# Optimization experiments

Hardware: AMD Instinct MI355X
Metric: run time of the kernel (lower is better)

Reference implementation:

```python
import jax, jax.numpy as jnp
import numpy as np

B = 8192   # particle ensemble (vmapped y0)
T = 64     # timesteps
D = 2      # data_size
W = 128    # width_size
CAP = 5.0  # cap() clamps trajectories to a bounded domain


def setup_inputs() -> dict:
    key = jax.random.key(0)
    ks = jax.random.split(key, 10)
    s_in = 1.0 / np.sqrt(D)
    s_h = 1.0 / np.sqrt(W)
    u = jax.random.uniform
    return {
        "ts": jnp.linspace(0.0, 1.0, T, dtype=jnp.float32),
        "y0": jax.random.normal(ks[0], (B, D), jnp.float32),
        "W1": u(ks[1], (W, D), jnp.float32, -s_in, s_in),
        "b1": u(ks[2], (W,), jnp.float32, -s_in, s_in),
        "W2": u(ks[3], (W, W), jnp.float32, -s_h, s_h),
        "b2": u(ks[4], (W,), jnp.float32, -s_h, s_h),
        "W3": u(ks[5], (W, W), jnp.float32, -s_h, s_h),
        "b3": u(ks[6], (W,), jnp.float32, -s_h, s_h),
        "W4": u(ks[7], (D, W), jnp.float32, -s_h, s_h),
        "b4": u(ks[8], (D,), jnp.float32, -s_h, s_h),
    }


def _func(y, W1, b1, W2, b2, W3, b3, W4, b4):
    # eqx.nn.MLP(data_size -> data_size, width_size, depth=3),
    # activation=leaky_relu, final_activation=identity. y: [B, D]
    h = jax.nn.leaky_relu(y @ W1.T + b1)
    h = jax.nn.leaky_relu(h @ W2.T + b2)
    h = jax.nn.leaky_relu(h @ W3.T + b3)
    return h @ W4.T + b4


def reference(ts, y0, W1, b1, W2, b2, W3, b3, W4, b4):
    # MultiTerm(drift, ODETerm(func)) with Euler on the uniform grid ts:
    #   y_{n+1} = y_n + dt_n * (drift(t_n, y_n) + func(t_n, y_n))
    # drift vector field: f(t, y) = -y
    dts = ts[1:] - ts[:-1]  # [T-1]

    def step(y, dt):
        dy = -y + _func(y, W1, b1, W2, b2, W3, b3, W4, b4)
        y_new = y + dt * dy
        return y_new, y_new

    _, ys_tail = jax.lax.scan(step, y0, dts)          # [T-1, B, D]
    ys = jnp.concatenate([y0[None], ys_tail], axis=0)  # [T, B, D] == solution.ys
    return jnp.clip(ys, -CAP, CAP)  # cap(solution.ys)
```

## Files before the change

kernel.cpp:

```cpp
#include <hip/hip_runtime.h>

#define NB 8192
#define NT 64
#define FCAP 5.0f

typedef unsigned int u32;
typedef float f32x4 __attribute__((ext_vector_type(4)));
typedef __bf16 bf16x8 __attribute__((ext_vector_type(8)));
typedef u32 u32x4 __attribute__((ext_vector_type(4)));
typedef u32 u32x2 __attribute__((ext_vector_type(2)));

static __device__ __forceinline__ u32 pk2(float lo, float hi) {
  u32 r;
  asm("v_cvt_pk_bf16_f32 %0, %1, %2" : "=v"(r) : "v"(lo), "v"(hi));
  return r;
}
static __device__ __forceinline__ float clipc(float a) { return fminf(fmaxf(a, -FCAP), FCAP); }

static __device__ __forceinline__ bf16x8 mkfrag(const float* __restrict__ p) {
  f32x4 a = *(const f32x4*)p, b = *(const f32x4*)(p + 4);
  u32x4 wv = {pk2(a[0], a[1]), pk2(a[2], a[3]), pk2(b[0], b[1]), pk2(b[2], b[3])};
  return __builtin_bit_cast(bf16x8, wv);
}

#define MFMA16(A, B, C) __builtin_amdgcn_mfma_f32_16x16x32_bf16(A, B, C, 0, 0, 0)

static __device__ __forceinline__ f32x4 lrelu4(f32x4 v) {
  return __builtin_elementwise_max(v, v * 0.01f);
}


__global__ __launch_bounds__(256, 2) void ode_kernel(
    const float* __restrict__ ts, const float* __restrict__ y0,
    const float* __restrict__ W1, const float* __restrict__ b1,
    const float* __restrict__ W2, const float* __restrict__ b2,
    const float* __restrict__ W3, const float* __restrict__ b3,
    const float* __restrict__ W4, const float* __restrict__ b4,
    float* __restrict__ out) {
  const int tid = threadIdx.x;
  const int wv = __builtin_amdgcn_readfirstlane(tid >> 6);
  const int l = tid & 63;
  const int g = l >> 4;
  const int c = l & 15;
  const int gp0 = blockIdx.x * 16;

  __shared__ alignas(16) u32 bufA[16 * 68];
  __shared__ alignas(16) u32 bufB[16 * 68];
  __shared__ alignas(16) float fbuf[16 * 20];

  bf16x8 aW2[2][4], aW3[2][4];
#pragma unroll
  for (int mt = 0; mt < 2; ++mt) {
    const int R = 32 * wv + 16 * mt + c;
#pragma unroll
    for (int kt = 0; kt < 4; ++kt) {
      aW2[mt][kt] = mkfrag(W2 + R * 128 + 32 * kt + 8 * g);
      aW3[mt][kt] = mkfrag(W3 + R * 128 + 32 * kt + 8 * g);
    }
  }
  bf16x8 aW1[2];
#pragma unroll
  for (int mt = 0; mt < 2; ++mt) {
    const int R = 32 * wv + 16 * mt + c;
    u32x4 f = {0, 0, 0, 0};
    if (g == 0) {
      f[0] = pk2(W1[2 * R], W1[2 * R + 1]);
      f[1] = pk2(b1[R], 0.f);
    }
    aW1[mt] = __builtin_bit_cast(bf16x8, f);
  }
  bf16x8 aW4;
  {
    u32x4 f = {0, 0, 0, 0};
    if (c < 2) {
      const float* s = W4 + c * 128 + 32 * wv + 8 * g;
      f32x4 a = *(const f32x4*)s, b = *(const f32x4*)(s + 4);
      f = (u32x4){pk2(a[0], a[1]), pk2(a[2], a[3]), pk2(b[0], b[1]), pk2(b[2], b[3])};
    }
    aW4 = __builtin_bit_cast(bf16x8, f);
  }
  f32x4 cb2[2], cb3[2];
#pragma unroll
  for (int mt = 0; mt < 2; ++mt) {
#pragma unroll
    for (int r = 0; r < 4; ++r) {
      const int row = 32 * wv + 16 * mt + 4 * g + r;
      cb2[mt][r] = b2[row];
      cb3[mt][r] = b3[row];
    }
  }
  const float b40 = b4[0], b41 = b4[1];

  float y1 = y0[(gp0 + c) * 2];
  float y2 = y0[(gp0 + c) * 2 + 1];

  if (wv == 0 && g == 0) {
    float2 st = {clipc(y1), clipc(y2)};
    *(float2*)(out + (gp0 + c) * 2) = st;
  }

  const f32x4 zero4 = {0.f, 0.f, 0.f, 0.f};
  const int wbase = 68 * c + 16 * wv + 2 * g;
  const int rbase = 68 * c + 4 * g;

#pragma unroll 1
  for (int t = 0; t < NT - 1; ++t) {
    const float dt = ts[t + 1] - ts[t];

    u32x4 byw = {0, 0, 0, 0};
    if (g == 0) {
      byw[0] = pk2(y1, y2);
      byw[1] = 0x3f80u;
    }
    const bf16x8 By = __builtin_bit_cast(bf16x8, byw);
    f32x4 C0 = lrelu4(MFMA16(aW1[0], By, zero4));
    f32x4 C1 = lrelu4(MFMA16(aW1[1], By, zero4));
    *(__shared__ u32x2*)&bufA[wbase]     = (u32x2){pk2(C0[0], C0[1]), pk2(C0[2], C0[3])};
    *(__shared__ u32x2*)&bufA[wbase + 8] = (u32x2){pk2(C1[0], C1[1]), pk2(C1[2], C1[3])};
    __syncthreads();

    {
      const bf16x8 q0 = __builtin_bit_cast(bf16x8, *(const __shared__ u32x4*)&bufA[rbase]);
      const bf16x8 q1 = __builtin_bit_cast(bf16x8, *(const __shared__ u32x4*)&bufA[rbase + 16]);
      const bf16x8 q2 = __builtin_bit_cast(bf16x8, *(const __shared__ u32x4*)&bufA[rbase + 32]);
      const bf16x8 q3 = __builtin_bit_cast(bf16x8, *(const __shared__ u32x4*)&bufA[rbase + 48]);
      f32x4 D0 = MFMA16(aW2[0][0], q0, cb2[0]);
      f32x4 D1 = MFMA16(aW2[1][0], q0, cb2[1]);
      f32x4 E0 = MFMA16(aW2[0][1], q1, zero4);
      f32x4 E1 = MFMA16(aW2[1][1], q1, zero4);
      D0 = MFMA16(aW2[0][2], q2, D0);
      D1 = MFMA16(aW2[1][2], q2, D1);
      E0 = MFMA16(aW2[0][3], q3, E0);
      E1 = MFMA16(aW2[1][3], q3, E1);
      C0 = lrelu4(D0 + E0);
      C1 = lrelu4(D1 + E1);
    }
    *(__shared__ u32x2*)&bufB[wbase]     = (u32x2){pk2(C0[0], C0[1]), pk2(C0[2], C0[3])};
    *(__shared__ u32x2*)&bufB[wbase + 8] = (u32x2){pk2(C1[0], C1[1]), pk2(C1[2], C1[3])};
    __syncthreads();

    {
      const bf16x8 q0 = __builtin_bit_cast(bf16x8, *(const __shared__ u32x4*)&bufB[rbase]);
      const bf16x8 q1 = __builtin_bit_cast(bf16x8, *(const __shared__ u32x4*)&bufB[rbase + 16]);
      const bf16x8 q2 = __builtin_bit_cast(bf16x8, *(const __shared__ u32x4*)&bufB[rbase + 32]);
      const bf16x8 q3 = __builtin_bit_cast(bf16x8, *(const __shared__ u32x4*)&bufB[rbase + 48]);
      f32x4 D0 = MFMA16(aW3[0][0], q0, cb3[0]);
      f32x4 D1 = MFMA16(aW3[1][0], q0, cb3[1]);
      f32x4 E0 = MFMA16(aW3[0][1], q1, zero4);
      f32x4 E1 = MFMA16(aW3[1][1], q1, zero4);
      D0 = MFMA16(aW3[0][2], q2, D0);
      D1 = MFMA16(aW3[1][2], q2, D1);
      E0 = MFMA16(aW3[0][3], q3, E0);
      E1 = MFMA16(aW3[1][3], q3, E1);
      C0 = lrelu4(D0 + E0);
      C1 = lrelu4(D1 + E1);
    }
    *(__shared__ u32x2*)&bufA[wbase]     = (u32x2){pk2(C0[0], C0[1]), pk2(C0[2], C0[3])};
    *(__shared__ u32x2*)&bufA[wbase + 8] = (u32x2){pk2(C1[0], C1[1]), pk2(C1[2], C1[3])};

    const bf16x8 q3v =
        __builtin_bit_cast(bf16x8, *(const __shared__ u32x4*)&bufA[rbase + 16 * wv]);
    f32x4 C4 = MFMA16(aW4, q3v, zero4);
    if (g == 0)
      *(__shared__ float2*)&fbuf[c * 20 + wv * 2] = (float2){C4[0], C4[1]};
    __syncthreads();

    const f32x4 pa = *(const __shared__ f32x4*)&fbuf[c * 20];
    const f32x4 pb = *(const __shared__ f32x4*)&fbuf[c * 20 + 4];
    const f32x4 s = pa + pb;
    const float f0 = b40 + s[0] + s[2];
    const float f1v = b41 + s[1] + s[3];
    y1 += dt * (f0 - y1);
    y2 += dt * (f1v - y2);

    if (wv == 0 && g == 0) {
      float2 st = {clipc(y1), clipc(y2)};
      *(float2*)(out + (t + 1) * (NB * 2) + (gp0 + c) * 2) = st;
    }
  }
}

extern "C" void kernel_launch(void* const* d_in, const int* in_sizes, int n_in,
                              void* d_out, int out_size, void* d_ws, size_t ws_size,
                              hipStream_t stream) {
  const float* ts = (const float*)d_in[0];
  const float* y0 = (const float*)d_in[1];
  const float* W1 = (const float*)d_in[2];
  const float* b1 = (const float*)d_in[3];
  const float* W2 = (const float*)d_in[4];
  const float* b2 = (const float*)d_in[5];
  const float* W3 = (const float*)d_in[6];
  const float* b3 = (const float*)d_in[7];
  const float* W4 = (const float*)d_in[8];
  const float* b4 = (const float*)d_in[9];

  ode_kernel<<<NB / 16, 256, 0, stream>>>(ts, y0, W1, b1, W2, b2, W3, b3, W4, b4,
                                          (float*)d_out);
}
```

Before: 67.72 us.

## Compute first and last MLP layers on VALU to drop a barrier

Layer 1 (D=2 inputs) is now computed redundantly per lane with FMAs directly into the bf16 B-fragment layout of the layer-2 MFMA, so the first shared-memory round trip and its barrier go away. The final 128->2 projection is done with scalar FMAs on the layer-3 accumulators plus cross-lane shuffles instead of another LDS write/read and an MFMA. This removes one __syncthreads and two LDS passes per timestep. In exchange each thread does 32 extra FMAs per step and holds about 112 more registers of layer-1 and layer-4 weights, which may hurt occupancy under the 2-blocks-per-SM launch bound.

```diff
diff --git a/kernel.cpp b/kernel.cpp
--- a/kernel.cpp
+++ b/kernel.cpp
@@ -28,7 +28,6 @@
 static __device__ __forceinline__ f32x4 lrelu4(f32x4 v) {
   return __builtin_elementwise_max(v, v * 0.01f);
 }
-
 
 __global__ __launch_bounds__(256, 2) void ode_kernel(
     const float* __restrict__ ts, const float* __restrict__ y0,
@@ -45,7 +44,6 @@
   const int gp0 = blockIdx.x * 16;
 
   __shared__ alignas(16) u32 bufA[16 * 68];
-  __shared__ alignas(16) u32 bufB[16 * 68];
   __shared__ alignas(16) float fbuf[16 * 20];
 
   bf16x8 aW2[2][4], aW3[2][4];
@@ -58,26 +56,26 @@
       aW3[mt][kt] = mkfrag(W3 + R * 128 + 32 * kt + 8 * g);
     }
   }
-  bf16x8 aW1[2];
+  float w1a[4][8], w1b[4][8], bb1[4][8];
+#pragma unroll
+  for (int kt = 0; kt < 4; ++kt) {
+#pragma unroll
+    for (int e = 0; e < 8; ++e) {
+      const int r = 32 * kt + 8 * g + e;
+      w1a[kt][e] = W1[2 * r];
+      w1b[kt][e] = W1[2 * r + 1];
+      bb1[kt][e] = b1[r];
+    }
+  }
+  float w40[8], w41[8];
 #pragma unroll
   for (int mt = 0; mt < 2; ++mt) {
-    const int R = 32 * wv + 16 * mt + c;
-    u32x4 f = {0, 0, 0, 0};
-    if (g == 0) {
-      f[0] = pk2(W1[2 * R], W1[2 * R + 1]);
-      f[1] = pk2(b1[R], 0.f);
-    }
-    aW1[mt] = __builtin_bit_cast(bf16x8, f);
-  }
-  bf16x8 aW4;
-  {
-    u32x4 f = {0, 0, 0, 0};
-    if (c < 2) {
-      const float* s = W4 + c * 128 + 32 * wv + 8 * g;
-      f32x4 a = *(const f32x4*)s, b = *(const f32x4*)(s + 4);
-      f = (u32x4){pk2(a[0], a[1]), pk2(a[2], a[3]), pk2(b[0], b[1]), pk2(b[2], b[3])};
-    }
-    aW4 = __builtin_bit_cast(bf16x8, f);
+#pragma unroll
+    for (int rr = 0; rr < 4; ++rr) {
+      const int row = 32 * wv + 16 * mt + 4 * g + rr;
+      w40[mt * 4 + rr] = W4[row];
+      w41[mt * 4 + rr] = W4[128 + row];
+    }
   }
   f32x4 cb2[2], cb3[2];
 #pragma unroll
@@ -107,23 +105,25 @@
   for (int t = 0; t < NT - 1; ++t) {
     const float dt = ts[t + 1] - ts[t];
 
-    u32x4 byw = {0, 0, 0, 0};
-    if (g == 0) {
-      byw[0] = pk2(y1, y2);
-      byw[1] = 0x3f80u;
-    }
-    const bf16x8 By = __builtin_bit_cast(bf16x8, byw);
-    f32x4 C0 = lrelu4(MFMA16(aW1[0], By, zero4));
-    f32x4 C1 = lrelu4(MFMA16(aW1[1], By, zero4));
-    *(__shared__ u32x2*)&bufA[wbase]     = (u32x2){pk2(C0[0], C0[1]), pk2(C0[2], C0[3])};
-    *(__shared__ u32x2*)&bufA[wbase + 8] = (u32x2){pk2(C1[0], C1[1]), pk2(C1[2], C1[3])};
-    __syncthreads();
-
+    u32x4 hb[4];
+#pragma unroll
+    for (int kt = 0; kt < 4; ++kt) {
+      float hv[8];
+#pragma unroll
+      for (int e = 0; e < 8; ++e) {
+        const float a = fmaf(w1a[kt][e], y1, fmaf(w1b[kt][e], y2, bb1[kt][e]));
+        hv[e] = fmaxf(a, 0.01f * a);
+      }
+      hb[kt] = (u32x4){pk2(hv[0], hv[1]), pk2(hv[2], hv[3]),
+                       pk2(hv[4], hv[5]), pk2(hv[6], hv[7])};
+    }
+
+    f32x4 C0, C1;
     {
-      const bf16x8 q0 = __builtin_bit_cast(bf16x8, *(const __shared__ u32x4*)&bufA[rbase]);
-      const bf16x8 q1 = __builtin_bit_cast(bf16x8, *(const __shared__ u32x4*)&bufA[rbase + 16]);
-      const bf16x8 q2 = __builtin_bit_cast(bf16x8, *(const __shared__ u32x4*)&bufA[rbase + 32]);
-      const bf16x8 q3 = __builtin_bit_cast(bf16x8, *(const __shared__ u32x4*)&bufA[rbase + 48]);
+      const bf16x8 q0 = __builtin_bit_cast(bf16x8, hb[0]);
+      const bf16x8 q1 = __builtin_bit_cast(bf16x8, hb[1]);
+      const bf16x8 q2 = __builtin_bit_cast(bf16x8, hb[2]);
+      const bf16x8 q3 = __builtin_bit_cast(bf16x8, hb[3]);
       f32x4 D0 = MFMA16(aW2[0][0], q0, cb2[0]);
       f32x4 D1 = MFMA16(aW2[1][0], q0, cb2[1]);
       f32x4 E0 = MFMA16(aW2[0][1], q1, zero4);
@@ -135,15 +135,16 @@
       C0 = lrelu4(D0 + E0);
       C1 = lrelu4(D1 + E1);
     }
-    *(__shared__ u32x2*)&bufB[wbase]     = (u32x2){pk2(C0[0], C0[1]), pk2(C0[2], C0[3])};
-    *(__shared__ u32x2*)&bufB[wbase + 8] = (u32x2){pk2(C1[0], C1[1]), pk2(C1[2], C1[3])};
+    *(__shared__ u32x2*)&bufA[wbase]     = (u32x2){pk2(C0[0], C0[1]), pk2(C0[2], C0[3])};
+    *(__shared__ u32x2*)&bufA[wbase + 8] = (u32x2){pk2(C1[0], C1[1]), pk2(C1[2], C1[3])};
     __syncthreads();
 
+    f32x4 H0, H1;
     {
-      const bf16x8 q0 = __builtin_bit_cast(bf16x8, *(const __shared__ u32x4*)&bufB[rbase]);
-      const bf16x8 q1 = __builtin_bit_cast(bf16x8, *(const __shared__ u32x4*)&bufB[rbase + 16]);
-      const bf16x8 q2 = __builtin_bit_cast(bf16x8, *(const __shared__ u32x4*)&bufB[rbase + 32]);
-      const bf16x8 q3 = __builtin_bit_cast(bf16x8, *(const __shared__ u32x4*)&bufB[rbase + 48]);
+      const bf16x8 q0 = __builtin_bit_cast(bf16x8, *(const __shared__ u32x4*)&bufA[rbase]);
+      const bf16x8 q1 = __builtin_bit_cast(bf16x8, *(const __shared__ u32x4*)&bufA[rbase + 16]);
+      const bf16x8 q2 = __builtin_bit_cast(bf16x8, *(const __shared__ u32x4*)&bufA[rbase + 32]);
+      const bf16x8 q3 = __builtin_bit_cast(bf16x8, *(const __shared__ u32x4*)&bufA[rbase + 48]);
       f32x4 D0 = MFMA16(aW3[0][0], q0, cb3[0]);
       f32x4 D1 = MFMA16(aW3[1][0], q0, cb3[1]);
       f32x4 E0 = MFMA16(aW3[0][1], q1, zero4);
@@ -152,26 +153,33 @@
       D1 = MFMA16(aW3[1][2], q2, D1);
       E0 = MFMA16(aW3[0][3], q3, E0);
       E1 = MFMA16(aW3[1][3], q3, E1);
-      C0 = lrelu4(D0 + E0);
-      C1 = lrelu4(D1 + E1);
-    }
-    *(__shared__ u32x2*)&bufA[wbase]     = (u32x2){pk2(C0[0], C0[1]), pk2(C0[2], C0[3])};
-    *(__shared__ u32x2*)&bufA[wbase + 8] = (u32x2){pk2(C1[0], C1[1]), pk2(C1[2], C1[3])};
-
-    const bf16x8 q3v =
-        __builtin_bit_cast(bf16x8, *(const __shared__ u32x4*)&bufA[rbase + 16 * wv]);
-    f32x4 C4 = MFMA16(aW4, q3v, zero4);
+      H0 = lrelu4(D0 + E0);
+      H1 = lrelu4(D1 + E1);
+    }
+
+    float f0 = 0.f, f1 = 0.f;
+#pragma unroll
+    for (int rr = 0; rr < 4; ++rr) {
+      f0 = fmaf(w40[rr], H0[rr], f0);
+      f0 = fmaf(w40[4 + rr], H1[rr], f0);
+      f1 = fmaf(w41[rr], H0[rr], f1);
+      f1 = fmaf(w41[4 + rr], H1[rr], f1);
+    }
+    f0 += __shfl_xor(f0, 16);
+    f1 += __shfl_xor(f1, 16);
+    f0 += __shfl_xor(f0, 32);
+    f1 += __shfl_xor(f1, 32);
     if (g == 0)
-      *(__shared__ float2*)&fbuf[c * 20 + wv * 2] = (float2){C4[0], C4[1]};
+      *(__shared__ float2*)&fbuf[c * 20 + wv * 2] = (float2){f0, f1};
     __syncthreads();
 
     const f32x4 pa = *(const __shared__ f32x4*)&fbuf[c * 20];
     const f32x4 pb = *(const __shared__ f32x4*)&fbuf[c * 20 + 4];
     const f32x4 s = pa + pb;
-    const float f0 = b40 + s[0] + s[2];
-    const float f1v = b41 + s[1] + s[3];
-    y1 += dt * (f0 - y1);
-    y2 += dt * (f1v - y2);
+    const float ft0 = b40 + s[0] + s[2];
+    const float ft1 = b41 + s[1] + s[3];
+    y1 += dt * (ft0 - y1);
+    y2 += dt * (ft1 - y2);
 
     if (wv == 0 && g == 0) {
       float2 st = {clipc(y1), clipc(y2)};
```

Measured after the change: 88.94 us. 1.31x slower.

## Pipeline MLP layers across warp groups with two interleaved particle sets

Applied to the files above, without the earlier changes.

Block grows to 512 threads handling 32 particles as two 16-particle sets. Waves 0-3 compute layers 1-2 and waves 4-7 compute layer 3 plus the output layer and Euler update, alternating sets so the two halves work concurrently. Each wave now holds only one layer's weights, which cuts register pressure. In exchange, every step needs four block-wide barriers, the grid has half as many blocks, and the final layer runs on a single wave.

```diff
diff --git a/kernel.cpp b/kernel.cpp
--- a/kernel.cpp
+++ b/kernel.cpp
@@ -29,8 +29,7 @@
   return __builtin_elementwise_max(v, v * 0.01f);
 }
 
-
-__global__ __launch_bounds__(256, 2) void ode_kernel(
+__global__ __launch_bounds__(512, 2) void ode_kernel(
     const float* __restrict__ ts, const float* __restrict__ y0,
     const float* __restrict__ W1, const float* __restrict__ b1,
     const float* __restrict__ W2, const float* __restrict__ b2,
@@ -42,88 +41,63 @@
   const int l = tid & 63;
   const int g = l >> 4;
   const int c = l & 15;
-  const int gp0 = blockIdx.x * 16;
-
-  __shared__ alignas(16) u32 bufA[16 * 68];
-  __shared__ alignas(16) u32 bufB[16 * 68];
-  __shared__ alignas(16) float fbuf[16 * 20];
-
-  bf16x8 aW2[2][4], aW3[2][4];
-#pragma unroll
-  for (int mt = 0; mt < 2; ++mt) {
-    const int R = 32 * wv + 16 * mt + c;
-#pragma unroll
-    for (int kt = 0; kt < 4; ++kt) {
-      aW2[mt][kt] = mkfrag(W2 + R * 128 + 32 * kt + 8 * g);
-      aW3[mt][kt] = mkfrag(W3 + R * 128 + 32 * kt + 8 * g);
-    }
+  const int gp0 = blockIdx.x * 32;
+
+  __shared__ alignas(16) u32 hb1[2][16 * 68];
+  __shared__ alignas(16) u32 hb2[2][16 * 68];
+  __shared__ alignas(16) u32 hb3[2][16 * 68];
+  __shared__ float yb[2][16][2];
+
+  const int rbase = 68 * c + 4 * g;
+  const f32x4 zero4 = {0.f, 0.f, 0.f, 0.f};
+
+  if ((wv == 0 || wv == 4) && g == 0) {
+    const int set = wv >> 2;
+    const float2 yv = *(const float2*)(y0 + (gp0 + 16 * set + c) * 2);
+    *(__shared__ float2*)&yb[set][c][0] = yv;
+    float2 st = {clipc(yv.x), clipc(yv.y)};
+    *(float2*)(out + (gp0 + 16 * set + c) * 2) = st;
   }
-  bf16x8 aW1[2];
-#pragma unroll
-  for (int mt = 0; mt < 2; ++mt) {
-    const int R = 32 * wv + 16 * mt + c;
-    u32x4 f = {0, 0, 0, 0};
-    if (g == 0) {
-      f[0] = pk2(W1[2 * R], W1[2 * R + 1]);
-      f[1] = pk2(b1[R], 0.f);
-    }
-    aW1[mt] = __builtin_bit_cast(bf16x8, f);
-  }
-  bf16x8 aW4;
-  {
-    u32x4 f = {0, 0, 0, 0};
-    if (c < 2) {
-      const float* s = W4 + c * 128 + 32 * wv + 8 * g;
-      f32x4 a = *(const f32x4*)s, b = *(const f32x4*)(s + 4);
-      f = (u32x4){pk2(a[0], a[1]), pk2(a[2], a[3]), pk2(b[0], b[1]), pk2(b[2], b[3])};
-    }
-    aW4 = __builtin_bit_cast(bf16x8, f);
-  }
-  f32x4 cb2[2], cb3[2];
-#pragma unroll
-  for (int mt = 0; mt < 2; ++mt) {
-#pragma unroll
-    for (int r = 0; r < 4; ++r) {
-      const int row = 32 * wv + 16 * mt + 4 * g + r;
-      cb2[mt][r] = b2[row];
-      cb3[mt][r] = b3[row];
-    }
-  }
-  const float b40 = b4[0], b41 = b4[1];
-
-  float y1 = y0[(gp0 + c) * 2];
-  float y2 = y0[(gp0 + c) * 2 + 1];
-
-  if (wv == 0 && g == 0) {
-    float2 st = {clipc(y1), clipc(y2)};
-    *(float2*)(out + (gp0 + c) * 2) = st;
-  }
-
-  const f32x4 zero4 = {0.f, 0.f, 0.f, 0.f};
-  const int wbase = 68 * c + 16 * wv + 2 * g;
-  const int rbase = 68 * c + 4 * g;
-
-#pragma unroll 1
-  for (int t = 0; t < NT - 1; ++t) {
-    const float dt = ts[t + 1] - ts[t];
-
-    u32x4 byw = {0, 0, 0, 0};
-    if (g == 0) {
-      byw[0] = pk2(y1, y2);
-      byw[1] = 0x3f80u;
-    }
-    const bf16x8 By = __builtin_bit_cast(bf16x8, byw);
-    f32x4 C0 = lrelu4(MFMA16(aW1[0], By, zero4));
-    f32x4 C1 = lrelu4(MFMA16(aW1[1], By, zero4));
-    *(__shared__ u32x2*)&bufA[wbase]     = (u32x2){pk2(C0[0], C0[1]), pk2(C0[2], C0[3])};
-    *(__shared__ u32x2*)&bufA[wbase + 8] = (u32x2){pk2(C1[0], C1[1]), pk2(C1[2], C1[3])};
-    __syncthreads();
-
-    {
-      const bf16x8 q0 = __builtin_bit_cast(bf16x8, *(const __shared__ u32x4*)&bufA[rbase]);
-      const bf16x8 q1 = __builtin_bit_cast(bf16x8, *(const __shared__ u32x4*)&bufA[rbase + 16]);
-      const bf16x8 q2 = __builtin_bit_cast(bf16x8, *(const __shared__ u32x4*)&bufA[rbase + 32]);
-      const bf16x8 q3 = __builtin_bit_cast(bf16x8, *(const __shared__ u32x4*)&bufA[rbase + 48]);
+
+  if (wv < 4) {
+    bf16x8 aW1[2], aW2[2][4];
+    f32x4 cb2[2];
+#pragma unroll
+    for (int mt = 0; mt < 2; ++mt) {
+      const int R = 32 * wv + 16 * mt + c;
+#pragma unroll
+      for (int kt = 0; kt < 4; ++kt)
+        aW2[mt][kt] = mkfrag(W2 + R * 128 + 32 * kt + 8 * g);
+      u32x4 f = {0, 0, 0, 0};
+      if (g == 0) {
+        f[0] = pk2(W1[2 * R], W1[2 * R + 1]);
+        f[1] = pk2(b1[R], 0.f);
+      }
+      aW1[mt] = __builtin_bit_cast(bf16x8, f);
+#pragma unroll
+      for (int r = 0; r < 4; ++r)
+        cb2[mt][r] = b2[32 * wv + 16 * mt + 4 * g + r];
+    }
+    const int wbase = 68 * c + 16 * wv + 2 * g;
+
+    auto UNIT_L1 = [&](int set) {
+      const float2 yv = *(__shared__ float2*)&yb[set][c][0];
+      u32x4 byw = {0, 0, 0, 0};
+      if (g == 0) {
+        byw[0] = pk2(yv.x, yv.y);
+        byw[1] = 0x3f80u;
+      }
+      const bf16x8 By = __builtin_bit_cast(bf16x8, byw);
+      f32x4 C0 = lrelu4(MFMA16(aW1[0], By, zero4));
+      f32x4 C1 = lrelu4(MFMA16(aW1[1], By, zero4));
+      *(__shared__ u32x2*)&hb1[set][wbase]     = (u32x2){pk2(C0[0], C0[1]), pk2(C0[2], C0[3])};
+      *(__shared__ u32x2*)&hb1[set][wbase + 8] = (u32x2){pk2(C1[0], C1[1]), pk2(C1[2], C1[3])};
+    };
+    auto UNIT_L2 = [&](int set) {
+      const bf16x8 q0 = __builtin_bit_cast(bf16x8, *(const __shared__ u32x4*)&hb1[set][rbase]);
+      const bf16x8 q1 = __builtin_bit_cast(bf16x8, *(const __shared__ u32x4*)&hb1[set][rbase + 16]);
+      const bf16x8 q2 = __builtin_bit_cast(bf16x8, *(const __shared__ u32x4*)&hb1[set][rbase + 32]);
+      const bf16x8 q3 = __builtin_bit_cast(bf16x8, *(const __shared__ u32x4*)&hb1[set][rbase + 48]);
       f32x4 D0 = MFMA16(aW2[0][0], q0, cb2[0]);
       f32x4 D1 = MFMA16(aW2[1][0], q0, cb2[1]);
       f32x4 E0 = MFMA16(aW2[0][1], q1, zero4);
@@ -132,18 +106,60 @@
       D1 = MFMA16(aW2[1][2], q2, D1);
       E0 = MFMA16(aW2[0][3], q3, E0);
       E1 = MFMA16(aW2[1][3], q3, E1);
-      C0 = lrelu4(D0 + E0);
-      C1 = lrelu4(D1 + E1);
-    }
-    *(__shared__ u32x2*)&bufB[wbase]     = (u32x2){pk2(C0[0], C0[1]), pk2(C0[2], C0[3])};
-    *(__shared__ u32x2*)&bufB[wbase + 8] = (u32x2){pk2(C1[0], C1[1]), pk2(C1[2], C1[3])};
-    __syncthreads();
-
-    {
-      const bf16x8 q0 = __builtin_bit_cast(bf16x8, *(const __shared__ u32x4*)&bufB[rbase]);
-      const bf16x8 q1 = __builtin_bit_cast(bf16x8, *(const __shared__ u32x4*)&bufB[rbase + 16]);
-      const bf16x8 q2 = __builtin_bit_cast(bf16x8, *(const __shared__ u32x4*)&bufB[rbase + 32]);
-      const bf16x8 q3 = __builtin_bit_cast(bf16x8, *(const __shared__ u32x4*)&bufB[rbase + 48]);
+      const f32x4 C0 = lrelu4(D0 + E0);
+      const f32x4 C1 = lrelu4(D1 + E1);
+      *(__shared__ u32x2*)&hb2[set][wbase]     = (u32x2){pk2(C0[0], C0[1]), pk2(C0[2], C0[3])};
+      *(__shared__ u32x2*)&hb2[set][wbase + 8] = (u32x2){pk2(C1[0], C1[1]), pk2(C1[2], C1[3])};
+    };
+
+    __syncthreads();
+    UNIT_L1(0);
+    __syncthreads();
+    UNIT_L2(0);
+    __syncthreads();
+#pragma unroll 1
+    for (int t = 0; t < NT - 1; ++t) {
+      UNIT_L1(1);
+      __syncthreads();
+      UNIT_L2(1);
+      __syncthreads();
+      if (t < NT - 2) UNIT_L1(0);
+      __syncthreads();
+      if (t < NT - 2) UNIT_L2(0);
+      __syncthreads();
+    }
+  } else {
+    const int s = wv - 4;
+    bf16x8 aW3[2][4], aW4[4];
+    f32x4 cb3[2];
+#pragma unroll
+    for (int mt = 0; mt < 2; ++mt) {
+      const int R = 32 * s + 16 * mt + c;
+#pragma unroll
+      for (int kt = 0; kt < 4; ++kt)
+        aW3[mt][kt] = mkfrag(W3 + R * 128 + 32 * kt + 8 * g);
+#pragma unroll
+      for (int r = 0; r < 4; ++r)
+        cb3[mt][r] = b3[32 * s + 16 * mt + 4 * g + r];
+    }
+#pragma unroll
+    for (int kt = 0; kt < 4; ++kt) {
+      u32x4 f = {0, 0, 0, 0};
+      if (c < 2) {
+        const float* p = W4 + c * 128 + 32 * kt + 8 * g;
+        f32x4 a = *(const f32x4*)p, b = *(const f32x4*)(p + 4);
+        f = (u32x4){pk2(a[0], a[1]), pk2(a[2], a[3]), pk2(b[0], b[1]), pk2(b[2], b[3])};
+      }
+      aW4[kt] = __builtin_bit_cast(bf16x8, f);
+    }
+    const float b40 = b4[0], b41 = b4[1];
+    const int wbase3 = 68 * c + 16 * s + 2 * g;
+
+    auto UNIT_L3 = [&](int set) {
+      const bf16x8 q0 = __builtin_bit_cast(bf16x8, *(const __shared__ u32x4*)&hb2[set][rbase]);
+      const bf16x8 q1 = __builtin_bit_cast(bf16x8, *(const __shared__ u32x4*)&hb2[set][rbase + 16]);
+      const bf16x8 q2 = __builtin_bit_cast(bf16x8, *(const __shared__ u32x4*)&hb2[set][rbase + 32]);
+      const bf16x8 q3 = __builtin_bit_cast(bf16x8, *(const __shared__ u32x4*)&hb2[set][rbase + 48]);
       f32x4 D0 = MFMA16(aW3[0][0], q0, cb3[0]);
       f32x4 D1 = MFMA16(aW3[1][0], q0, cb3[1]);
       f32x4 E0 = MFMA16(aW3[0][1], q1, zero4);
@@ -152,30 +168,48 @@
       D1 = MFMA16(aW3[1][2], q2, D1);
       E0 = MFMA16(aW3[0][3], q3, E0);
       E1 = MFMA16(aW3[1][3], q3, E1);
-      C0 = lrelu4(D0 + E0);
-      C1 = lrelu4(D1 + E1);
-    }
-    *(__shared__ u32x2*)&bufA[wbase]     = (u32x2){pk2(C0[0], C0[1]), pk2(C0[2], C0[3])};
-    *(__shared__ u32x2*)&bufA[wbase + 8] = (u32x2){pk2(C1[0], C1[1]), pk2(C1[2], C1[3])};
-
-    const bf16x8 q3v =
-        __builtin_bit_cast(bf16x8, *(const __shared__ u32x4*)&bufA[rbase + 16 * wv]);
-    f32x4 C4 = MFMA16(aW4, q3v, zero4);
-    if (g == 0)
-      *(__shared__ float2*)&fbuf[c * 20 + wv * 2] = (float2){C4[0], C4[1]};
-    __syncthreads();
-
-    const f32x4 pa = *(const __shared__ f32x4*)&fbuf[c * 20];
-    const f32x4 pb = *(const __shared__ f32x4*)&fbuf[c * 20 + 4];
-    const f32x4 s = pa + pb;
-    const float f0 = b40 + s[0] + s[2];
-    const float f1v = b41 + s[1] + s[3];
-    y1 += dt * (f0 - y1);
-    y2 += dt * (f1v - y2);
-
-    if (wv == 0 && g == 0) {
-      float2 st = {clipc(y1), clipc(y2)};
-      *(float2*)(out + (t + 1) * (NB * 2) + (gp0 + c) * 2) = st;
+      const f32x4 C0 = lrelu4(D0 + E0);
+      const f32x4 C1 = lrelu4(D1 + E1);
+      *(__shared__ u32x2*)&hb3[set][wbase3]     = (u32x2){pk2(C0[0], C0[1]), pk2(C0[2], C0[3])};
+      *(__shared__ u32x2*)&hb3[set][wbase3 + 8] = (u32x2){pk2(C1[0], C1[1]), pk2(C1[2], C1[3])};
+    };
+    auto UNIT_L4E = [&](int set, float dt, int t) {
+      if (wv == 4) {
+        const bf16x8 q0 = __builtin_bit_cast(bf16x8, *(const __shared__ u32x4*)&hb3[set][rbase]);
+        const bf16x8 q1 = __builtin_bit_cast(bf16x8, *(const __shared__ u32x4*)&hb3[set][rbase + 16]);
+        const bf16x8 q2 = __builtin_bit_cast(bf16x8, *(const __shared__ u32x4*)&hb3[set][rbase + 32]);
+        const bf16x8 q3 = __builtin_bit_cast(bf16x8, *(const __shared__ u32x4*)&hb3[set][rbase + 48]);
+        f32x4 D = MFMA16(aW4[0], q0, zero4);
+        f32x4 E = MFMA16(aW4[1], q1, zero4);
+        D = MFMA16(aW4[2], q2, D);
+        E = MFMA16(aW4[3], q3, E);
+        const f32x4 C4 = D + E;
+        if (g == 0) {
+          const float2 yo = *(__shared__ float2*)&yb[set][c][0];
+          const float f0 = C4[0] + b40, f1 = C4[1] + b41;
+          const float y1n = yo.x + dt * (f0 - yo.x);
+          const float y2n = yo.y + dt * (f1 - yo.y);
+          *(__shared__ float2*)&yb[set][c][0] = (float2){y1n, y2n};
+          float2 st = {clipc(y1n), clipc(y2n)};
+          *(float2*)(out + (t + 1) * (NB * 2) + (gp0 + 16 * set + c) * 2) = st;
+        }
+      }
+    };
+
+    __syncthreads();
+    __syncthreads();
+    __syncthreads();
+#pragma unroll 1
+    for (int t = 0; t < NT - 1; ++t) {
+      const float dt = ts[t + 1] - ts[t];
+      UNIT_L3(0);
+      __syncthreads();
+      UNIT_L4E(0, dt, t);
+      __syncthreads();
+      UNIT_L3(1);
+      __syncthreads();
+      UNIT_L4E(1, dt, t);
+      __syncthreads();
     }
   }
 }
@@ -194,6 +228,6 @@
   const float* W4 = (const float*)d_in[8];
   const float* b4 = (const float*)d_in[9];
 
-  ode_kernel<<<NB / 16, 256, 0, stream>>>(ts, y0, W1, b1, W2, b2, W3, b3, W4, b4,
+  ode_kernel<<<NB / 32, 512, 0, stream>>>(ts, y0, W1, b1, W2, b2, W3, b3, W4, b4,
                                           (float*)d_out);
 }
```

Result: slower. 70.67 us (+4.4%).
